# Optimization experiments

Measured on AMD Instinct MI355X. Metric: run time of the kernel, lower is better.

The kernel has to match this reference:

```python
import jax, jax.numpy as jnp
import numpy as np

B, S, D_IN, H, D_OUT = 2048, 16, 512, 1024, 64

def _lin_init(key, fan_in, fan_out):
    k1, k2 = jax.random.split(key)
    bound = 1.0 / np.sqrt(fan_in)
    W = jax.random.uniform(k1, (fan_in, fan_out), jnp.float32, -bound, bound)
    b = jax.random.uniform(k2, (fan_out,), jnp.float32, -bound, bound)
    return W, b

def setup_inputs() -> dict:
    key = jax.random.key(0)
    ks = jax.random.split(key, 7)
    x = jax.random.normal(ks[0], (B, S, D_IN), jnp.float32)
    Wi, bi = _lin_init(ks[1], D_IN, H)
    W1, b1 = _lin_init(ks[2], H, H)
    W2, b2 = _lin_init(ks[3], H, H)
    W3, b3 = _lin_init(ks[4], H, H)
    Wo1, bo1 = _lin_init(ks[5], H, H // 2)
    Wo2, bo2 = _lin_init(ks[6], H // 2, D_OUT)
    return {"x": x, "Wi": Wi, "bi": bi, "W1": W1, "b1": b1, "W2": W2, "b2": b2,
            "W3": W3, "b3": b3, "Wo1": Wo1, "bo1": bo1, "Wo2": Wo2, "bo2": bo2}

def reference(x, Wi, bi, W1, b1, W2, b2, W3, b3, Wo1, bo1, Wo2, bo2):
    seq_len = x.shape[1]
    dt = 1.0 / (seq_len - 1)  # t = linspace(0, 1, seq_len)

    def f(h):
        h = jax.nn.gelu(h @ W1 + b1, approximate=False)
        h = jax.nn.gelu(h @ W2 + b2, approximate=False)
        h = jax.nn.gelu(h @ W3 + b3, approximate=False)
        return h

    h0 = x[:, 0, :] @ Wi + bi  # [B, H]

    def rk4_38_step(h, _):  # torchdiffeq fixed-grid rk4 uses the 3/8 rule
        k1 = f(h)
        k2 = f(h + dt * k1 / 3.0)
        k3 = f(h + dt * (k2 - k1 / 3.0))
        k4 = f(h + dt * (k1 - k2 + k3))
        return h + dt * (k1 + 3.0 * k2 + 3.0 * k3 + k4) / 8.0, None

    h_final, _ = jax.lax.scan(rk4_38_step, h0, None, length=seq_len - 1)
    out = jax.nn.gelu(h_final @ Wo1 + bo1, approximate=False) @ Wo2 + bo2
    return out
```

## Files before the change

kernel.cpp:

```cpp
#include <hip/hip_runtime.h>
#include <hip/hip_bf16.h>
#include <math.h>

typedef __attribute__((ext_vector_type(8))) short bf16x8;
typedef __attribute__((ext_vector_type(4))) float f32x4;

#define EPI_T   0
#define EPI_H0  1
#define EPI_K1  2
#define EPI_K2  3
#define EPI_K3  4
#define EPI_K4  5
#define EPI_OUT 6

static __device__ __forceinline__ unsigned short f2bf(float f) {
  unsigned int u = __float_as_uint(f);
  u += 0x7FFFu + ((u >> 16) & 1u);
  return (unsigned short)(u >> 16);
}
static __device__ __forceinline__ float bf2f(unsigned short s) {
  return __uint_as_float(((unsigned int)s) << 16);
}
static __device__ __forceinline__ float gelu_f(float x) {
  return 0.5f * x * (1.0f + erff(x * 0.70710678118654752f));
}

typedef __attribute__((address_space(3))) unsigned int lds_u32;
typedef const __attribute__((address_space(1))) unsigned int glb_u32;
static __device__ __forceinline__ void gl_lds16(const unsigned short* g, unsigned short* l) {
  __builtin_amdgcn_global_load_lds((glb_u32*)g, (lds_u32*)l, 16, 0, 0);
}

template<int EPI>
__global__ __launch_bounds__(256)
void gemm_k(const unsigned short* __restrict__ A,
            const unsigned short* __restrict__ Wt,
            const float* __restrict__ bias,
            void* __restrict__ outp,
            unsigned short* __restrict__ ob2,
            const float* __restrict__ hF,
            float* __restrict__ huF,
            const unsigned short* __restrict__ k1p,
            const unsigned short* __restrict__ k2p,
            float dt, int N, int K, int nwg)
{
  __shared__ __attribute__((aligned(16))) unsigned short As[2][128][64];
  __shared__ __attribute__((aligned(16))) unsigned short Bs[2][64][64];

  int bid = blockIdx.x;
  const int cpx = nwg >> 3;
  const int wid = (bid & 7) * cpx + (bid >> 3);
  const int nbx = N >> 6;
  const int bx = wid % nbx, by = wid / nbx;
  const int brow = by << 7, bcol = bx << 6;

  const int tid = threadIdx.x;
  const int lane = tid & 63;
  const int wv = tid >> 6;
  const int wr = wv >> 1, wc = wv & 1;
  const int l15 = lane & 15, l4 = lane >> 4;
  const int lr = lane >> 3;
  const int sc = (lane & 7) ^ lr;
  const int KT = K >> 6;

  f32x4 acc[4][2];
  const f32x4 zf = {0.f, 0.f, 0.f, 0.f};
#pragma unroll
  for (int m = 0; m < 4; ++m)
#pragma unroll
    for (int n = 0; n < 2; ++n) acc[m][n] = zf;

  auto STAGE = [&](int buf, int kt) {
    const int kof = kt << 6;
#pragma unroll
    for (int c = 0; c < 4; ++c) {
      const int r0 = c * 32 + wv * 8;
      gl_lds16(A + (size_t)(brow + r0 + lr) * K + kof + sc * 8, &As[buf][r0][0]);
    }
#pragma unroll
    for (int c = 0; c < 2; ++c) {
      const int r0 = c * 32 + wv * 8;
      gl_lds16(Wt + (size_t)(bcol + r0 + lr) * K + kof + sc * 8, &Bs[buf][r0][0]);
    }
  };

  auto COMP = [&](int buf) {
#pragma unroll
    for (int ks = 0; ks < 2; ++ks) {
      const int cb = ks * 4 + l4;
      const int ch = cb ^ (l15 & 7);
      bf16x8 af[4], bg[2];
#pragma unroll
      for (int m = 0; m < 4; ++m)
        af[m] = *(const bf16x8*)&As[buf][wr * 64 + m * 16 + l15][ch * 8];
#pragma unroll
      for (int n = 0; n < 2; ++n)
        bg[n] = *(const bf16x8*)&Bs[buf][wc * 32 + n * 16 + l15][ch * 8];
#pragma unroll
      for (int m = 0; m < 4; ++m)
#pragma unroll
        for (int n = 0; n < 2; ++n)
          acc[m][n] = __builtin_amdgcn_mfma_f32_16x16x32_bf16(af[m], bg[n], acc[m][n], 0, 0, 0);
    }
  };

  STAGE(0, 0);
  int b = 0;
  for (int kt = 0; kt < KT; ++kt) {
    __syncthreads();
    if (kt + 1 < KT) STAGE(b ^ 1, kt + 1);
    COMP(b);
    b ^= 1;
  }

  const float dt3 = dt * (1.f / 3.f), dt8 = dt * 0.125f, dt38 = dt * 0.375f;
#pragma unroll
  for (int n = 0; n < 2; ++n) {
    const int col = bcol + wc * 32 + n * 16 + l15;
    const float bv = bias[col];
#pragma unroll
    for (int m = 0; m < 4; ++m) {
      const int r0 = brow + wr * 64 + m * 16 + l4 * 4;
#pragma unroll
      for (int r = 0; r < 4; ++r) {
        const int row = r0 + r;
        const float a = acc[m][n][r] + bv;
        const size_t ix = (size_t)row * N + col;
        const size_t ih = (size_t)row * 1024 + col;
        if constexpr (EPI == EPI_T) {
          ((unsigned short*)outp)[ix] = f2bf(gelu_f(a));
        } else if constexpr (EPI == EPI_H0) {
          ((float*)outp)[ix] = a;
          ob2[ix] = f2bf(a);
        } else if constexpr (EPI == EPI_K1) {
          const float k1 = gelu_f(a);
          const float h = hF[ih];
          ((unsigned short*)outp)[ih] = f2bf(k1);
          huF[ih] = h + dt8 * k1;
          ob2[ih] = f2bf(h + dt3 * k1);
        } else if constexpr (EPI == EPI_K2) {
          const float k2 = gelu_f(a);
          const float h = hF[ih];
          const float k1 = bf2f(k1p[ih]);
          ((unsigned short*)outp)[ih] = f2bf(k2);
          huF[ih] += dt38 * k2;
          ob2[ih] = f2bf(h - dt3 * k1 + dt * k2);
        } else if constexpr (EPI == EPI_K3) {
          const float k3 = gelu_f(a);
          const float h = hF[ih];
          const float k1 = bf2f(k1p[ih]);
          const float k2 = bf2f(k2p[ih]);
          huF[ih] += dt38 * k3;
          ob2[ih] = f2bf(h + dt * (k1 - k2 + k3));
        } else if constexpr (EPI == EPI_K4) {
          const float k4 = gelu_f(a);
          const float hn = huF[ih] + dt8 * k4;
          ((float*)outp)[ih] = hn;
          ob2[ih] = f2bf(hn);
        } else {
          ((float*)outp)[ix] = a;
        }
      }
    }
  }
}

__global__ void transpose_k(const float* __restrict__ W, unsigned short* __restrict__ Wt,
                            int K, int N) {
  __shared__ float tile[32][33];
  const int n0 = blockIdx.x * 32, k0 = blockIdx.y * 32;
  const int lx = threadIdx.x, ly = threadIdx.y;
#pragma unroll
  for (int r = ly; r < 32; r += 8)
    tile[r][lx] = W[(size_t)(k0 + r) * N + n0 + lx];
  __syncthreads();
#pragma unroll
  for (int r = ly; r < 32; r += 8)
    Wt[(size_t)(n0 + r) * K + k0 + lx] = f2bf(tile[lx][r]);
}

__global__ void convx_k(const float* __restrict__ x, unsigned short* __restrict__ xb) {
  const int r = blockIdx.x;
  const int c = threadIdx.x << 3;
  const float* s = x + (size_t)r * 8192 + c;
  f32x4 u0 = *(const f32x4*)s;
  f32x4 u1 = *(const f32x4*)(s + 4);
  union { unsigned short q[8]; bf16x8 v; } t;
#pragma unroll
  for (int j = 0; j < 4; ++j) { t.q[j] = f2bf(u0[j]); t.q[4 + j] = f2bf(u1[j]); }
  *(bf16x8*)(xb + (size_t)r * 512 + c) = t.v;
}

template<int EPI>
static inline void G(hipStream_t st, const void* A, const unsigned short* Wt,
                     const float* bias, void* out, void* ob2,
                     const float* hF, float* huF,
                     const unsigned short* k1p, const unsigned short* k2p,
                     float dt, int N, int K) {
  const int nwg = (2048 / 128) * (N / 64);
  gemm_k<EPI><<<nwg, 256, 0, st>>>((const unsigned short*)A, Wt, bias, out,
                                   (unsigned short*)ob2, hF, huF, k1p, k2p, dt, N, K, nwg);
}

extern "C" void kernel_launch(void* const* d_in, const int* in_sizes, int n_in,
                              void* d_out, int out_size, void* d_ws, size_t ws_size,
                              hipStream_t stream) {
  const float* x   = (const float*)d_in[0];
  const float* Wi  = (const float*)d_in[1];
  const float* bi  = (const float*)d_in[2];
  const float* W1  = (const float*)d_in[3];
  const float* b1  = (const float*)d_in[4];
  const float* W2  = (const float*)d_in[5];
  const float* b2  = (const float*)d_in[6];
  const float* W3  = (const float*)d_in[7];
  const float* b3  = (const float*)d_in[8];
  const float* Wo1 = (const float*)d_in[9];
  const float* bo1 = (const float*)d_in[10];
  const float* Wo2 = (const float*)d_in[11];
  const float* bo2 = (const float*)d_in[12];

  char* ws = (char*)d_ws;
  unsigned short* Wti  = (unsigned short*)(ws + (0ull  << 20));
  unsigned short* Wt1  = (unsigned short*)(ws + (1ull  << 20));
  unsigned short* Wt2  = (unsigned short*)(ws + (3ull  << 20));
  unsigned short* Wt3  = (unsigned short*)(ws + (5ull  << 20));
  unsigned short* Wto1 = (unsigned short*)(ws + (7ull  << 20));
  unsigned short* Wto2 = (unsigned short*)(ws + (8ull  << 20));
  float*          h    = (float*)(ws + (9ull  << 20));
  float*          hu   = (float*)(ws + (17ull << 20));
  unsigned short* xb   = (unsigned short*)hu;
  unsigned short* k1b  = (unsigned short*)(ws + (25ull << 20));
  unsigned short* o1b  = k1b;
  unsigned short* k2b  = (unsigned short*)(ws + (29ull << 20));
  unsigned short* t1b  = (unsigned short*)(ws + (33ull << 20));
  unsigned short* t2b  = (unsigned short*)(ws + (37ull << 20));
  unsigned short* cA   = (unsigned short*)(ws + (41ull << 20));
  unsigned short* hb   = (unsigned short*)(ws + (45ull << 20));

  dim3 tb(32, 8);
  transpose_k<<<dim3(1024 / 32,  512 / 32), tb, 0, stream>>>(Wi,  Wti,  512, 1024);
  transpose_k<<<dim3(1024 / 32, 1024 / 32), tb, 0, stream>>>(W1,  Wt1, 1024, 1024);
  transpose_k<<<dim3(1024 / 32, 1024 / 32), tb, 0, stream>>>(W2,  Wt2, 1024, 1024);
  transpose_k<<<dim3(1024 / 32, 1024 / 32), tb, 0, stream>>>(W3,  Wt3, 1024, 1024);
  transpose_k<<<dim3( 512 / 32, 1024 / 32), tb, 0, stream>>>(Wo1, Wto1, 1024, 512);
  transpose_k<<<dim3(  64 / 32,  512 / 32), tb, 0, stream>>>(Wo2, Wto2,  512,  64);
  convx_k<<<2048, 64, 0, stream>>>(x, xb);

  const float dt = 1.0f / 15.0f;

  G<EPI_H0>(stream, xb, Wti, bi, h, hb, nullptr, nullptr, nullptr, nullptr, dt, 1024, 512);

  for (int s = 0; s < 15; ++s) {
    G<EPI_T >(stream, hb,  Wt1, b1, t1b, nullptr, nullptr, nullptr, nullptr, nullptr, dt, 1024, 1024);
    G<EPI_T >(stream, t1b, Wt2, b2, t2b, nullptr, nullptr, nullptr, nullptr, nullptr, dt, 1024, 1024);
    G<EPI_K1>(stream, t2b, Wt3, b3, k1b, cA, h, hu, nullptr, nullptr, dt, 1024, 1024);
    G<EPI_T >(stream, cA,  Wt1, b1, t1b, nullptr, nullptr, nullptr, nullptr, nullptr, dt, 1024, 1024);
    G<EPI_T >(stream, t1b, Wt2, b2, t2b, nullptr, nullptr, nullptr, nullptr, nullptr, dt, 1024, 1024);
    G<EPI_K2>(stream, t2b, Wt3, b3, k2b, cA, h, hu, k1b, nullptr, dt, 1024, 1024);
    G<EPI_T >(stream, cA,  Wt1, b1, t1b, nullptr, nullptr, nullptr, nullptr, nullptr, dt, 1024, 1024);
    G<EPI_T >(stream, t1b, Wt2, b2, t2b, nullptr, nullptr, nullptr, nullptr, nullptr, dt, 1024, 1024);
    G<EPI_K3>(stream, t2b, Wt3, b3, nullptr, cA, h, hu, k1b, k2b, dt, 1024, 1024);
    G<EPI_T >(stream, cA,  Wt1, b1, t1b, nullptr, nullptr, nullptr, nullptr, nullptr, dt, 1024, 1024);
    G<EPI_T >(stream, t1b, Wt2, b2, t2b, nullptr, nullptr, nullptr, nullptr, nullptr, dt, 1024, 1024);
    G<EPI_K4>(stream, t2b, Wt3, b3, h, hb, nullptr, hu, nullptr, nullptr, dt, 1024, 1024);
  }

  G<EPI_T  >(stream, hb,  Wto1, bo1, o1b, nullptr, nullptr, nullptr, nullptr, nullptr, dt, 512, 1024);
  G<EPI_OUT>(stream, o1b, Wto2, bo2, d_out, nullptr, nullptr, nullptr, nullptr, nullptr, dt, 64, 512);
}
```

Baseline: 3.754 ms.

## Shrink GEMM tile to 64x64 and load weight fragments directly from global

The block tile goes from 128x64 to 64x64, which doubles the workgroup count. Each wave now computes a 32x32 sub-tile. The weight (B) operand is no longer staged through LDS: each lane reads its bf16x8 fragments straight from global memory into registers every k-step, and only the activation tile stays double-buffered in LDS. The aim is more parallelism across CUs for these small-M GEMMs and less LDS traffic, at the cost of uncoalesced, unpipelined global B loads and lower arithmetic intensity per tile.

```diff
diff --git a/kernel.cpp b/kernel.cpp
--- a/kernel.cpp
+++ b/kernel.cpp
@@ -44,15 +44,14 @@
             const unsigned short* __restrict__ k2p,
             float dt, int N, int K, int nwg)
 {
-  __shared__ __attribute__((aligned(16))) unsigned short As[2][128][64];
-  __shared__ __attribute__((aligned(16))) unsigned short Bs[2][64][64];
-
-  int bid = blockIdx.x;
+  __shared__ __attribute__((aligned(16))) unsigned short As[2][64][64];
+
+  const int bid = blockIdx.x;
   const int cpx = nwg >> 3;
   const int wid = (bid & 7) * cpx + (bid >> 3);
   const int nbx = N >> 6;
   const int bx = wid % nbx, by = wid / nbx;
-  const int brow = by << 7, bcol = bx << 6;
+  const int brow = by << 6, bcol = bx << 6;
 
   const int tid = threadIdx.x;
   const int lane = tid & 63;
@@ -63,44 +62,22 @@
   const int sc = (lane & 7) ^ lr;
   const int KT = K >> 6;
 
-  f32x4 acc[4][2];
+  f32x4 acc[2][2];
   const f32x4 zf = {0.f, 0.f, 0.f, 0.f};
 #pragma unroll
-  for (int m = 0; m < 4; ++m)
+  for (int m = 0; m < 2; ++m)
 #pragma unroll
     for (int n = 0; n < 2; ++n) acc[m][n] = zf;
+
+  const unsigned short* pB0 = Wt + (size_t)(bcol + wc * 32 + l15) * K + l4 * 8;
+  const unsigned short* pB1 = pB0 + (size_t)16 * K;
 
   auto STAGE = [&](int buf, int kt) {
     const int kof = kt << 6;
 #pragma unroll
-    for (int c = 0; c < 4; ++c) {
+    for (int c = 0; c < 2; ++c) {
       const int r0 = c * 32 + wv * 8;
       gl_lds16(A + (size_t)(brow + r0 + lr) * K + kof + sc * 8, &As[buf][r0][0]);
-    }
-#pragma unroll
-    for (int c = 0; c < 2; ++c) {
-      const int r0 = c * 32 + wv * 8;
-      gl_lds16(Wt + (size_t)(bcol + r0 + lr) * K + kof + sc * 8, &Bs[buf][r0][0]);
-    }
-  };
-
-  auto COMP = [&](int buf) {
-#pragma unroll
-    for (int ks = 0; ks < 2; ++ks) {
-      const int cb = ks * 4 + l4;
-      const int ch = cb ^ (l15 & 7);
-      bf16x8 af[4], bg[2];
-#pragma unroll
-      for (int m = 0; m < 4; ++m)
-        af[m] = *(const bf16x8*)&As[buf][wr * 64 + m * 16 + l15][ch * 8];
-#pragma unroll
-      for (int n = 0; n < 2; ++n)
-        bg[n] = *(const bf16x8*)&Bs[buf][wc * 32 + n * 16 + l15][ch * 8];
-#pragma unroll
-      for (int m = 0; m < 4; ++m)
-#pragma unroll
-        for (int n = 0; n < 2; ++n)
-          acc[m][n] = __builtin_amdgcn_mfma_f32_16x16x32_bf16(af[m], bg[n], acc[m][n], 0, 0, 0);
     }
   };
 
@@ -109,7 +86,22 @@
   for (int kt = 0; kt < KT; ++kt) {
     __syncthreads();
     if (kt + 1 < KT) STAGE(b ^ 1, kt + 1);
-    COMP(b);
+    bf16x8 bg0[2], bg1[2];
+#pragma unroll
+    for (int ks = 0; ks < 2; ++ks) {
+      bg0[ks] = *(const bf16x8*)(pB0 + kt * 64 + ks * 32);
+      bg1[ks] = *(const bf16x8*)(pB1 + kt * 64 + ks * 32);
+    }
+#pragma unroll
+    for (int ks = 0; ks < 2; ++ks) {
+      const int ch = ((ks * 4 + l4) ^ (l15 & 7)) * 8;
+      bf16x8 af0 = *(const bf16x8*)&As[b][wr * 32 + l15][ch];
+      bf16x8 af1 = *(const bf16x8*)&As[b][wr * 32 + 16 + l15][ch];
+      acc[0][0] = __builtin_amdgcn_mfma_f32_16x16x32_bf16(af0, bg0[ks], acc[0][0], 0, 0, 0);
+      acc[0][1] = __builtin_amdgcn_mfma_f32_16x16x32_bf16(af0, bg1[ks], acc[0][1], 0, 0, 0);
+      acc[1][0] = __builtin_amdgcn_mfma_f32_16x16x32_bf16(af1, bg0[ks], acc[1][0], 0, 0, 0);
+      acc[1][1] = __builtin_amdgcn_mfma_f32_16x16x32_bf16(af1, bg1[ks], acc[1][1], 0, 0, 0);
+    }
     b ^= 1;
   }
 
@@ -119,8 +111,8 @@
     const int col = bcol + wc * 32 + n * 16 + l15;
     const float bv = bias[col];
 #pragma unroll
-    for (int m = 0; m < 4; ++m) {
-      const int r0 = brow + wr * 64 + m * 16 + l4 * 4;
+    for (int m = 0; m < 2; ++m) {
+      const int r0 = brow + wr * 32 + m * 16 + l4 * 4;
 #pragma unroll
       for (int r = 0; r < 4; ++r) {
         const int row = r0 + r;
@@ -197,7 +189,7 @@
                      const float* hF, float* huF,
                      const unsigned short* k1p, const unsigned short* k2p,
                      float dt, int N, int K) {
-  const int nwg = (2048 / 128) * (N / 64);
+  const int nwg = (2048 / 64) * (N / 64);
   gemm_k<EPI><<<nwg, 256, 0, st>>>((const unsigned short*)A, Wt, bias, out,
                                    (unsigned short*)ob2, hF, huF, k1p, k2p, dt, N, K, nwg);
 }
```

Result: slower. 3.993 ms (+6.4%).
